# Kernel optimization log

Measured on AMD Instinct MI355X. Metric: run time of the kernel, lower is better.

Reference implementation:

```python
import jax, jax.numpy as jnp
import numpy as np

DK = 64  # head dim = n_features // n_heads = 512 // 8


def setup_inputs() -> dict:
    key = jax.random.key(0)
    ks = jax.random.split(key, 6)
    B, N, D = 2, 4096, 512
    feature = jax.random.normal(ks[0], (B, N, D), dtype=jnp.float32)
    Sh = jax.random.normal(ks[1], (B, N, N), dtype=jnp.float32)
    Sw = jax.random.normal(ks[2], (B, N, N), dtype=jnp.float32)
    # torch Linear weights are [out, in]; xavier-uniform init
    lim = np.sqrt(6.0 / (D + DK)).astype(np.float32)
    wq_w = jax.random.uniform(ks[3], (DK, D), jnp.float32, -lim, lim)
    wk_w = jax.random.uniform(ks[4], (DK, D), jnp.float32, -lim, lim)
    wv_w = jax.random.uniform(ks[5], (DK, D), jnp.float32, -lim, lim)
    zb = jnp.zeros((DK,), jnp.float32)
    return {"feature": feature, "Sh": Sh, "Sw": Sw,
            "wq_w": wq_w, "wq_b": zb, "wk_w": wk_w, "wk_b": zb,
            "wv_w": wv_w, "wv_b": zb}


def reference(feature, Sh, Sw, wq_w, wq_b, wk_w, wk_b, wv_w, wv_b):
    # Linear projections (torch: x @ W.T + b)
    Q = jnp.einsum('bnd,kd->bnk', feature, wq_w) + wq_b  # [B,N,dk]
    K = jnp.einsum('bnd,kd->bnk', feature, wk_w) + wk_b  # [B,N,dk]
    V = jnp.einsum('bnd,kd->bnk', feature, wv_w) + wv_b  # [B,N,dv]
    sqrt_dk = jnp.sqrt(jnp.float32(Q.shape[-1]))
    # scores = (QK^T + Sh + Sw) / sqrt(dk)  -- biases added BEFORE scaling,
    # exactly as in attnFunc
    A = (jnp.einsum('bqk,bnk->bqn', Q, K) + Sh + Sw) / sqrt_dk  # [B,N,N]
    A = jax.nn.softmax(A, axis=-1)
    return jnp.einsum('bqn,bnk->bqk', A, V)  # [B,N,dv]
```

## Files before the change

kernel.cpp:

```cpp
#include <hip/hip_runtime.h>
#include <hip/hip_bf16.h>


typedef short bf16x8 __attribute__((ext_vector_type(8)));
typedef short bf16x4 __attribute__((ext_vector_type(4)));
typedef float f32x4  __attribute__((ext_vector_type(4)));

#if __has_builtin(__builtin_amdgcn_exp2f)
#define EXP2F(x) __builtin_amdgcn_exp2f(x)
#else
#define EXP2F(x) exp2f(x)
#endif
#if __has_builtin(__builtin_amdgcn_rcpf)
#define RCPF(x) __builtin_amdgcn_rcpf(x)
#else
#define RCPF(x) (1.0f / (x))
#endif

__device__ __forceinline__ f32x4 mfma16(bf16x8 a, bf16x8 b, f32x4 c) {
  return __builtin_amdgcn_mfma_f32_16x16x32_bf16(a, b, c, 0, 0, 0);
}
__device__ __forceinline__ short f2b(float x) {
  __hip_bfloat16 h = __float2bfloat16(x);
  return __builtin_bit_cast(short, h);
}
__device__ __forceinline__ void split_hl(float x, short& h, short& l) {
  __hip_bfloat16 bh = __float2bfloat16(x);
  h = __builtin_bit_cast(short, bh);
  l = f2b(x - __bfloat162float(bh));
}

__global__ void wcvt_kernel(const float* __restrict__ wq, const float* __restrict__ wk,
                            const float* __restrict__ wv,
                            short* __restrict__ wh, short* __restrict__ wl) {
  int idx = (blockIdx.x * 256 + threadIdx.x) * 4;
  int p = idx >> 15;
  int off = idx & 32767;
  const float* src = (p == 0) ? wq : (p == 1) ? wk : wv;
  f32x4 v = *(const f32x4*)(src + off);
  bf16x4 h, l;
#pragma unroll
  for (int j = 0; j < 4; ++j) { short hh, ll; split_hl(v[j], hh, ll); h[j] = hh; l[j] = ll; }
  *(bf16x4*)(wh + p * 32768 + off) = h;
  *(bf16x4*)(wl + p * 32768 + off) = l;
}

__global__ __launch_bounds__(256) void proj_kernel(
    const float* __restrict__ feat, const short* __restrict__ wh, const short* __restrict__ wl,
    const float* __restrict__ bq, const float* __restrict__ bk, const float* __restrict__ bv,
    short* __restrict__ Qh, short* __restrict__ Ql,
    short* __restrict__ Kh, short* __restrict__ Kl, short* __restrict__ Vt) {
  const int lane = threadIdx.x & 63, wave = threadIdx.x >> 6;
  const int lq = lane & 15, quad = lane >> 4;
  const int wid = blockIdx.x * 4 + wave;
  const int p = wid >> 9, rg = wid & 511;
  const int rbase = rg * 16;
  const float Cs = 0.18033688011112042f;

  f32x4 acc[4];
#pragma unroll
  for (int t = 0; t < 4; ++t) acc[t] = (f32x4){0.f, 0.f, 0.f, 0.f};

  const float* frow = feat + (size_t)(rbase + lq) * 512 + quad * 8;
  const int wrow = p * 64;
  for (int ks = 0; ks < 16; ++ks) {
    f32x4 f0 = *(const f32x4*)(frow + ks * 32);
    f32x4 f1 = *(const f32x4*)(frow + ks * 32 + 4);
    bf16x8 fh, fl;
#pragma unroll
    for (int j = 0; j < 4; ++j) {
      short hh, ll;
      split_hl(f0[j], hh, ll); fh[j] = hh; fl[j] = ll;
      split_hl(f1[j], hh, ll); fh[j + 4] = hh; fl[j + 4] = ll;
    }
#pragma unroll
    for (int t = 0; t < 4; ++t) {
      const int wo = (wrow + t * 16 + lq) * 512 + ks * 32 + quad * 8;
      bf16x8 wfh = *(const bf16x8*)(wh + wo);
      bf16x8 wfl = *(const bf16x8*)(wl + wo);
      acc[t] = mfma16(fh, wfh, acc[t]);
      acc[t] = mfma16(fl, wfh, acc[t]);
      acc[t] = mfma16(fh, wfl, acc[t]);
    }
  }
  const int b = rbase >> 12, rloc = rbase & 4095;
  if (p == 0) {
#pragma unroll
    for (int t = 0; t < 4; ++t) {
      const int dk = t * 16 + lq;
      const float bb = bq[dk];
#pragma unroll
      for (int r = 0; r < 4; ++r) {
        const int row = rbase + 4 * quad + r;
        short h, l;
        split_hl((acc[t][r] + bb) * Cs, h, l);
        Qh[row * 64 + dk] = h; Ql[row * 64 + dk] = l;
      }
    }
  } else if (p == 1) {
#pragma unroll
    for (int t = 0; t < 4; ++t) {
      const int dk = t * 16 + lq;
      const float bb = bk[dk];
#pragma unroll
      for (int r = 0; r < 4; ++r) {
        const int row = rbase + 4 * quad + r;
        short h, l;
        split_hl(acc[t][r] + bb, h, l);
        Kh[row * 64 + dk] = h; Kl[row * 64 + dk] = l;
      }
    }
  } else {
#pragma unroll
    for (int t = 0; t < 4; ++t) {
      const int dk = t * 16 + lq;
      const float bb = bv[dk];
      bf16x4 vpack;
#pragma unroll
      for (int r = 0; r < 4; ++r) vpack[r] = f2b(acc[t][r] + bb);
      *(bf16x4*)(Vt + (size_t)(b * 64 + dk) * 4096 + rloc + 4 * quad) = vpack;
    }
  }
}

__global__ __launch_bounds__(256, 4) void attn_kernel(
    const float* __restrict__ Sh, const float* __restrict__ Sw,
    const short* __restrict__ Qh, const short* __restrict__ Ql,
    const short* __restrict__ Kh, const short* __restrict__ Kl,
    const short* __restrict__ Vt,
    float* __restrict__ Opart, float* __restrict__ lpart) {
  __shared__ short Plds[4][16][72];
  const int bid = blockIdx.x;
  const int sp = bid & 7, qt = (bid >> 3) & 63, b = bid >> 9;
  const int tid = threadIdx.x;
  const int wave = tid >> 6, lane = tid & 63, lq = lane & 15, quad = lane >> 4;
  const int qbase = qt * 64 + wave * 16;
  const float Cs = 0.18033688011112042f;

  const int qidx = (b * 4096 + qbase + lq) * 64 + quad * 8;
  const bf16x8 qfh0 = *(const bf16x8*)(Qh + qidx);
  const bf16x8 qfh1 = *(const bf16x8*)(Qh + qidx + 32);
  const bf16x8 qfl0 = *(const bf16x8*)(Ql + qidx);
  const bf16x8 qfl1 = *(const bf16x8*)(Ql + qidx + 32);

  f32x4 accO[4];
#pragma unroll
  for (int u = 0; u < 4; ++u) accO[u] = (f32x4){0.f, 0.f, 0.f, 0.f};
  float lsum = 0.f;
  const size_t qrowOff = (size_t)(b * 4096 + qbase + lq) * 4096;
  short* pw = &Plds[wave][0][0];
  const short* vbase = Vt + (size_t)b * 64 * 4096;

  for (int it = 0; it < 8; ++it) {
    const int kb = sp * 512 + it * 64;
    bf16x8 kh0[4], kh1[4], kl0[4], kl1[4];
#pragma unroll
    for (int t = 0; t < 4; ++t) {
      const int kidx = (b * 4096 + kb + t * 16 + lq) * 64 + quad * 8;
      kh0[t] = *(const bf16x8*)(Kh + kidx);
      kh1[t] = *(const bf16x8*)(Kh + kidx + 32);
      kl0[t] = *(const bf16x8*)(Kl + kidx);
      kl1[t] = *(const bf16x8*)(Kl + kidx + 32);
    }
    f32x4 bsh[4], bsw[4];
#pragma unroll
    for (int t = 0; t < 4; ++t) {
      const size_t bi = qrowOff + kb + 16 * t + 4 * quad;
      bsh[t] = __builtin_nontemporal_load((const f32x4*)(Sh + bi));
      bsw[t] = __builtin_nontemporal_load((const f32x4*)(Sw + bi));
    }
    f32x4 accS[4];
#pragma unroll
    for (int t = 0; t < 4; ++t) accS[t] = (f32x4){0.f, 0.f, 0.f, 0.f};
#pragma unroll
    for (int t = 0; t < 4; ++t) {
      accS[t] = mfma16(kh0[t], qfh0, accS[t]);
      accS[t] = mfma16(kh1[t], qfh1, accS[t]);
      accS[t] = mfma16(kh0[t], qfl0, accS[t]);
      accS[t] = mfma16(kh1[t], qfl1, accS[t]);
      accS[t] = mfma16(kl0[t], qfh0, accS[t]);
      accS[t] = mfma16(kl1[t], qfh1, accS[t]);
    }
#pragma unroll
    for (int t = 0; t < 4; ++t) {
      bf16x4 pk;
#pragma unroll
      for (int r = 0; r < 4; ++r) {
        float s = fmaf(bsh[t][r] + bsw[t][r], Cs, accS[t][r]);
        float p = EXP2F(s);
        lsum += p;
        pk[r] = f2b(p);
      }
      *(bf16x4*)(pw + lq * 72 + 16 * t + 4 * quad) = pk;
    }
#pragma unroll
    for (int c = 0; c < 2; ++c) {
      const bf16x8 pa = *(const bf16x8*)(pw + lq * 72 + c * 32 + quad * 8);
#pragma unroll
      for (int u = 0; u < 4; ++u) {
        const bf16x8 vf = *(const bf16x8*)(vbase + (size_t)(u * 16 + lq) * 4096 + kb + c * 32 + quad * 8);
        accO[u] = mfma16(pa, vf, accO[u]);
      }
    }
  }
  lsum += __shfl_xor(lsum, 16, 64);
  lsum += __shfl_xor(lsum, 32, 64);

  const int orowW = sp * 8192 + b * 4096 + qbase;
  if (quad == 0) lpart[orowW + lq] = lsum;
#pragma unroll
  for (int u = 0; u < 4; ++u)
#pragma unroll
    for (int r = 0; r < 4; ++r)
      Opart[(size_t)(orowW + 4 * quad + r) * 64 + u * 16 + lq] = accO[u][r];
}

__global__ void combine_kernel(const float* __restrict__ Opart, const float* __restrict__ lpart,
                               float* __restrict__ out) {
  const int g = blockIdx.x * 256 + threadIdx.x;
  const int row = g >> 4;
  f32x4 o = (f32x4){0.f, 0.f, 0.f, 0.f};
  float l = 0.f;
#pragma unroll
  for (int s = 0; s < 8; ++s) {
    o += __builtin_nontemporal_load((const f32x4*)(Opart + (size_t)s * 524288 + g * 4));
    l += lpart[s * 8192 + row];
  }
  const float rl = RCPF(l);
  *(f32x4*)(out + g * 4) = o * rl;
}

extern "C" void kernel_launch(void* const* d_in, const int* in_sizes, int n_in,
                              void* d_out, int out_size, void* d_ws, size_t ws_size,
                              hipStream_t stream) {
  const float* feature = (const float*)d_in[0];
  const float* Sh = (const float*)d_in[1];
  const float* Sw = (const float*)d_in[2];
  const float* wq = (const float*)d_in[3];
  const float* bq = (const float*)d_in[4];
  const float* wk = (const float*)d_in[5];
  const float* bk = (const float*)d_in[6];
  const float* wv = (const float*)d_in[7];
  const float* bv = (const float*)d_in[8];

  char* ws = (char*)d_ws;
  const size_t MB = 1u << 20;
  short* Qh = (short*)(ws + 0 * MB);
  short* Ql = (short*)(ws + 1 * MB);
  short* Kh = (short*)(ws + 2 * MB);
  short* Kl = (short*)(ws + 3 * MB);
  short* Vt = (short*)(ws + 4 * MB);
  short* wh = (short*)(ws + 5 * MB);
  short* wl = (short*)(ws + 5 * MB + 262144);
  float* lpart = (float*)(ws + 5 * MB + 524288);
  float* Opart = (float*)(ws + 6 * MB);

  wcvt_kernel<<<96, 256, 0, stream>>>(wq, wk, wv, wh, wl);
  proj_kernel<<<384, 256, 0, stream>>>(feature, wh, wl, bq, bk, bv, Qh, Ql, Kh, Kl, Vt);
  attn_kernel<<<1024, 256, 0, stream>>>(Sh, Sw, Qh, Ql, Kh, Kl, Vt, Opart, lpart);
  combine_kernel<<<512, 256, 0, stream>>>(Opart, lpart, (float*)d_out);
}
```

Measured before the change: 398.5 us.

## Prestage Sh+Sw bias into LDS as bf16 and drop K low-part MFMAs

Each wave now streams its full 16x512 slice of Sh and Sw up front with coalesced row-contiguous loads. It stores the pre-scaled sum as bf16 in a new LDS buffer and reads it back inside the key loop, instead of doing strided per-iteration global loads. Separately, it drops the Kl low-part MFMAs and loads, cutting QK^T compute. The larger LDS footprint (about 66KB per block) may lower occupancy, and storing the bias and K in bf16 loses precision before the exponent.

```diff
diff --git a/kernel.cpp b/kernel.cpp
--- a/kernel.cpp
+++ b/kernel.cpp
@@ -23,6 +23,9 @@
 __device__ __forceinline__ short f2b(float x) {
   __hip_bfloat16 h = __float2bfloat16(x);
   return __builtin_bit_cast(short, h);
+}
+__device__ __forceinline__ float b2f(short s) {
+  return __bfloat162float(__builtin_bit_cast(__hip_bfloat16, s));
 }
 __device__ __forceinline__ void split_hl(float x, short& h, short& l) {
   __hip_bfloat16 bh = __float2bfloat16(x);
@@ -126,10 +129,10 @@
 __global__ __launch_bounds__(256, 4) void attn_kernel(
     const float* __restrict__ Sh, const float* __restrict__ Sw,
     const short* __restrict__ Qh, const short* __restrict__ Ql,
-    const short* __restrict__ Kh, const short* __restrict__ Kl,
-    const short* __restrict__ Vt,
+    const short* __restrict__ Kh, const short* __restrict__ Vt,
     float* __restrict__ Opart, float* __restrict__ lpart) {
   __shared__ short Plds[4][16][72];
+  __shared__ short BiasLds[4][16][520];
   const int bid = blockIdx.x;
   const int sp = bid & 7, qt = (bid >> 3) & 63, b = bid >> 9;
   const int tid = threadIdx.x;
@@ -143,31 +146,47 @@
   const bf16x8 qfl0 = *(const bf16x8*)(Ql + qidx);
   const bf16x8 qfl1 = *(const bf16x8*)(Ql + qidx + 32);
 
+  short* bw = &BiasLds[wave][0][0];
+  const float* shp = Sh + (size_t)(b * 4096 + qbase) * 4096 + sp * 512;
+  const float* swp = Sw + (size_t)(b * 4096 + qbase) * 4096 + sp * 512;
+  f32x4 sa[4], sc[4];
+#pragma unroll
+  for (int i = 0; i < 4; ++i) {
+    const size_t off = (size_t)(i >> 1) * 4096 + (i & 1) * 256 + lane * 4;
+    sa[i] = __builtin_nontemporal_load((const f32x4*)(shp + off));
+    sc[i] = __builtin_nontemporal_load((const f32x4*)(swp + off));
+  }
+#pragma unroll 4
+  for (int i = 0; i < 32; ++i) {
+    const int sl = i & 3;
+    f32x4 s = (sa[sl] + sc[sl]) * Cs;
+    bf16x4 pk;
+#pragma unroll
+    for (int j = 0; j < 4; ++j) pk[j] = f2b(s[j]);
+    *(bf16x4*)(bw + (i >> 1) * 520 + (i & 1) * 256 + lane * 4) = pk;
+    if (i + 4 < 32) {
+      const int in = i + 4;
+      const size_t off = (size_t)(in >> 1) * 4096 + (in & 1) * 256 + lane * 4;
+      sa[sl] = __builtin_nontemporal_load((const f32x4*)(shp + off));
+      sc[sl] = __builtin_nontemporal_load((const f32x4*)(swp + off));
+    }
+  }
+
   f32x4 accO[4];
 #pragma unroll
   for (int u = 0; u < 4; ++u) accO[u] = (f32x4){0.f, 0.f, 0.f, 0.f};
   float lsum = 0.f;
-  const size_t qrowOff = (size_t)(b * 4096 + qbase + lq) * 4096;
   short* pw = &Plds[wave][0][0];
   const short* vbase = Vt + (size_t)b * 64 * 4096;
 
   for (int it = 0; it < 8; ++it) {
     const int kb = sp * 512 + it * 64;
-    bf16x8 kh0[4], kh1[4], kl0[4], kl1[4];
+    bf16x8 kh0[4], kh1[4];
 #pragma unroll
     for (int t = 0; t < 4; ++t) {
       const int kidx = (b * 4096 + kb + t * 16 + lq) * 64 + quad * 8;
       kh0[t] = *(const bf16x8*)(Kh + kidx);
       kh1[t] = *(const bf16x8*)(Kh + kidx + 32);
-      kl0[t] = *(const bf16x8*)(Kl + kidx);
-      kl1[t] = *(const bf16x8*)(Kl + kidx + 32);
-    }
-    f32x4 bsh[4], bsw[4];
-#pragma unroll
-    for (int t = 0; t < 4; ++t) {
-      const size_t bi = qrowOff + kb + 16 * t + 4 * quad;
-      bsh[t] = __builtin_nontemporal_load((const f32x4*)(Sh + bi));
-      bsw[t] = __builtin_nontemporal_load((const f32x4*)(Sw + bi));
     }
     f32x4 accS[4];
 #pragma unroll
@@ -178,15 +197,14 @@
       accS[t] = mfma16(kh1[t], qfh1, accS[t]);
       accS[t] = mfma16(kh0[t], qfl0, accS[t]);
       accS[t] = mfma16(kh1[t], qfl1, accS[t]);
-      accS[t] = mfma16(kl0[t], qfh0, accS[t]);
-      accS[t] = mfma16(kl1[t], qfh1, accS[t]);
-    }
-#pragma unroll
-    for (int t = 0; t < 4; ++t) {
+    }
+#pragma unroll
+    for (int t = 0; t < 4; ++t) {
+      const bf16x4 bb = *(const bf16x4*)(bw + lq * 520 + it * 64 + 16 * t + 4 * quad);
       bf16x4 pk;
 #pragma unroll
       for (int r = 0; r < 4; ++r) {
-        float s = fmaf(bsh[t][r] + bsw[t][r], Cs, accS[t][r]);
+        float s = accS[t][r] + b2f(bb[r]);
         float p = EXP2F(s);
         lsum += p;
         pk[r] = f2b(p);
@@ -257,6 +275,6 @@
 
   wcvt_kernel<<<96, 256, 0, stream>>>(wq, wk, wv, wh, wl);
   proj_kernel<<<384, 256, 0, stream>>>(feature, wh, wl, bq, bk, bv, Qh, Ql, Kh, Kl, Vt);
-  attn_kernel<<<1024, 256, 0, stream>>>(Sh, Sw, Qh, Ql, Kh, Kl, Vt, Opart, lpart);
+  attn_kernel<<<1024, 256, 0, stream>>>(Sh, Sw, Qh, Ql, Kh, Vt, Opart, lpart);
   combine_kernel<<<512, 256, 0, stream>>>(Opart, lpart, (float*)d_out);
 }
```

Result: faster. 375.3 us (-5.8%).
